# Kernel tuning notes

Hardware: AMD Instinct MI355X
Metric: run time of the kernel (lower is better)

The kernel has to match this reference:

```python
import jax, jax.numpy as jnp
import numpy as np

NUM_HEADS = 8


def setup_inputs() -> dict:
    key = jax.random.key(0)
    ks = jax.random.split(key, 8)
    B, C, H, W = 8, 512, 64, 64
    s = 1.0 / np.sqrt(C)
    return {
        "guide": jax.random.normal(ks[0], (B, C), dtype=jnp.float32),
        "hidden_rep": jax.random.normal(ks[1], (B, C, H, W), dtype=jnp.float32),
        "Wq": jax.random.normal(ks[2], (C, C), dtype=jnp.float32) * s,
        "bq": jnp.zeros((C,), dtype=jnp.float32),
        "Wk": jax.random.normal(ks[3], (C, C), dtype=jnp.float32) * s,
        "bk": jnp.zeros((C,), dtype=jnp.float32),
        "Wv": jax.random.normal(ks[4], (C, C), dtype=jnp.float32) * s,
        "bv": jnp.zeros((C,), dtype=jnp.float32),
    }


def reference(guide, hidden_rep, Wq, bq, Wk, bk, Wv, bv):
    B, C, H, W = hidden_rep.shape
    nh = NUM_HEADS
    d = C // nh
    scale = 1.0 / (d ** 0.5)

    # hidden_rep: [B,C,H,W] -> [B, HW, C] (token-major, matching torch permute+reshape)
    hr = hidden_rep.transpose(0, 2, 3, 1).reshape(B, H * W, C)

    # guide is broadcast identically over all HW positions in the original;
    # the linear commutes with the broadcast, so compute once then broadcast.
    q_row = guide @ Wq.T + bq                                   # [B, C]
    q_tok = jnp.broadcast_to(q_row[:, None, :], (B, H * W, C))  # [B, HW, C]
    k_tok = hr @ Wk.T + bk                                      # [B, HW, C]
    v_tok = hr @ Wv.T + bv                                      # [B, HW, C]

    # Faithful replication of torch split_heads: view [B,HW,C] as [B,nh,d,H,W]
    # (this scrambles spatial/channel axes exactly as the original does),
    # then permute to [B, nh, H, W, d].
    def split_heads(x):
        return x.reshape(B, nh, d, H, W).transpose(0, 1, 3, 4, 2)

    q = split_heads(q_tok)  # [B, nh, H, W, d]
    k = split_heads(k_tok)
    v = split_heads(v_tok)

    # Row-wise attention: softmax over the width axis only.
    scores = jnp.einsum('bnhqd,bnhkd->bnhqk', q, k) * scale  # [B, nh, H, W, W]
    weights = jax.nn.softmax(scores, axis=-1)
    attended = jnp.einsum('bnhqk,bnhkd->bnhqd', weights, v)  # [B, nh, H, W, d]

    # permute(0,1,4,2,3) -> [B, nh, d, H, W] -> [B, C, H, W]
    return attended.transpose(0, 1, 4, 2, 3).reshape(B, C, H, W)
```

## Files before the change

kernel.cpp:

```cpp
#include <hip/hip_runtime.h>
#include <hip/hip_bf16.h>
#include <stdint.h>


typedef __attribute__((ext_vector_type(8))) short bf16x8_t;
typedef __attribute__((ext_vector_type(4))) float f32x4_t;

__device__ __forceinline__ unsigned short f2bf(float f) {
  unsigned int u = __float_as_uint(f);
  u += 0x7FFFu + ((u >> 16) & 1u);
  return (unsigned short)(u >> 16);
}

__device__ __forceinline__ void gload16(const void* g, void* lds) {
  __builtin_amdgcn_global_load_lds(
      (const __attribute__((address_space(1))) unsigned int*)g,
      (__attribute__((address_space(3))) unsigned int*)lds, 16, 0, 0);
}

__global__ __launch_bounds__(256) void k_trans(const float* __restrict__ hid,
                                               unsigned short* __restrict__ XT,
                                               float* __restrict__ hrsum,
                                               const float* __restrict__ Wv,
                                               unsigned short* __restrict__ Wvb) {
  int bid = blockIdx.x;
  int tid = threadIdx.x;
  if (bid >= 512) {
    int blk = bid - 512;
#pragma unroll
    for (int i = 0; i < 16; ++i) {
      int idx = blk * 4096 + i * 256 + tid;
      float4 v = ((const float4*)Wv)[idx];
      ushort4 o;
      o.x = f2bf(v.x); o.y = f2bf(v.y); o.z = f2bf(v.z); o.w = f2bf(v.w);
      ((ushort4*)Wvb)[idx] = o;
    }
    return;
  }
  int cb = bid & 7, n = (bid >> 3) & 7, b = bid >> 6;
  __shared__ float T[64][65];
  __shared__ float hsred[64][8];

  for (int i = tid; i < 512; i += 256) ((float*)hsred)[i] = 0.f;

  float part[4][4];
#pragma unroll
  for (int m = 0; m < 4; ++m)
#pragma unroll
    for (int i = 0; i < 4; ++i) part[m][i] = 0.f;

  const int f4 = tid & 15;
  const int r0 = tid >> 4;
  const float* srcbase = hid + (size_t)(b * 512 + cb * 64) * 4096 + n * 512;
  unsigned short* xtbase = XT + (size_t)(b * 8 + n) * 512 * 512 + cb * 64;

  for (int jc = 0; jc < 8; ++jc) {
    __syncthreads();
#pragma unroll
    for (int m = 0; m < 4; ++m) {
      int r = r0 + 16 * m;
      float4 v = *(const float4*)(srcbase + (size_t)r * 4096 + jc * 64 + f4 * 4);
      T[r][f4 * 4 + 0] = v.x;  T[r][f4 * 4 + 1] = v.y;
      T[r][f4 * 4 + 2] = v.z;  T[r][f4 * 4 + 3] = v.w;
      part[m][0] += v.x; part[m][1] += v.y; part[m][2] += v.z; part[m][3] += v.w;
    }
    __syncthreads();
#pragma unroll
    for (int p = 0; p < 2; ++p) {
      int jl = (tid >> 3) + p * 32;
      int o = tid & 7;
      unsigned short t0 = f2bf(T[o * 8 + 0][jl]);
      unsigned short t1 = f2bf(T[o * 8 + 1][jl]);
      unsigned short t2 = f2bf(T[o * 8 + 2][jl]);
      unsigned short t3 = f2bf(T[o * 8 + 3][jl]);
      unsigned short t4 = f2bf(T[o * 8 + 4][jl]);
      unsigned short t5 = f2bf(T[o * 8 + 5][jl]);
      unsigned short t6 = f2bf(T[o * 8 + 6][jl]);
      unsigned short t7 = f2bf(T[o * 8 + 7][jl]);
      uint4 pk;
      pk.x = (unsigned)t0 | ((unsigned)t1 << 16);
      pk.y = (unsigned)t2 | ((unsigned)t3 << 16);
      pk.z = (unsigned)t4 | ((unsigned)t5 << 16);
      pk.w = (unsigned)t6 | ((unsigned)t7 << 16);
      *(uint4*)(xtbase + (size_t)(jc * 64 + jl) * 512 + o * 8) = pk;
    }
  }
  __syncthreads();
  {
    int gbase = (tid & 1) * 4;
#pragma unroll
    for (int m = 0; m < 4; ++m) {
      int r = r0 + 16 * m;
#pragma unroll
      for (int i = 0; i < 4; ++i) atomicAdd(&hsred[r][gbase + i], part[m][i]);
    }
  }
  __syncthreads();
  float* hout = hrsum + (size_t)(b * 8 + n) * 8 * 512 + cb * 64;
  for (int i = tid; i < 512; i += 256) {
    int g = i >> 6, r = i & 63;
    hout[(size_t)g * 512 + r] = hsred[r][g];
  }
}

__global__ __launch_bounds__(256) void k_k2(const float* __restrict__ hrsum,
                                            const float* __restrict__ Wk,
                                            const float* __restrict__ bk,
                                            const float* __restrict__ guide,
                                            const float* __restrict__ Wq,
                                            const float* __restrict__ bq,
                                            float* __restrict__ K2,
                                            float* __restrict__ qs) {
  int bid = blockIdx.x;
  int rt = bid >> 4, ct = bid & 15;
  bool isQ = (rt == 16);
  const float* A = isQ ? guide : (hrsum + (size_t)rt * 32 * 512);
  const float* Bm = isQ ? Wq : Wk;
  int arows = isQ ? 8 : 32;
  int tid = threadIdx.x;
  __shared__ float Ah[32][36];
  __shared__ float Bh[32][36];
  int r = tid >> 3, f = tid & 7;
  int oy = (tid >> 4) * 2, ox = (tid & 15) * 2;
  float a00 = 0.f, a01 = 0.f, a10 = 0.f, a11 = 0.f;

  for (int kc = 0; kc < 16; ++kc) {
    __syncthreads();
    float4 av = (r < arows) ? *(const float4*)(A + (size_t)r * 512 + kc * 32 + f * 4)
                            : make_float4(0.f, 0.f, 0.f, 0.f);
    *(float4*)(&Ah[r][f * 4]) = av;
    float4 bv = *(const float4*)(Bm + (size_t)(ct * 32 + r) * 512 + kc * 32 + f * 4);
    *(float4*)(&Bh[r][f * 4]) = bv;
    __syncthreads();
#pragma unroll
    for (int kk = 0; kk < 32; kk += 4) {
      float4 x0 = *(float4*)(&Ah[oy][kk]);
      float4 x1 = *(float4*)(&Ah[oy + 1][kk]);
      float4 y0 = *(float4*)(&Bh[ox][kk]);
      float4 y1 = *(float4*)(&Bh[ox + 1][kk]);
      a00 += x0.x * y0.x + x0.y * y0.y + x0.z * y0.z + x0.w * y0.w;
      a01 += x0.x * y1.x + x0.y * y1.y + x0.z * y1.z + x0.w * y1.w;
      a10 += x1.x * y0.x + x1.y * y0.y + x1.z * y0.z + x1.w * y0.w;
      a11 += x1.x * y1.x + x1.y * y1.y + x1.z * y1.z + x1.w * y1.w;
    }
  }
  int c0 = ct * 32 + ox;
  if (!isQ) {
    int row0 = rt * 32 + oy;
    K2[(size_t)row0 * 512 + c0]           = a00 + 64.f * bk[c0];
    K2[(size_t)row0 * 512 + c0 + 1]       = a01 + 64.f * bk[c0 + 1];
    K2[(size_t)(row0 + 1) * 512 + c0]     = a10 + 64.f * bk[c0];
    K2[(size_t)(row0 + 1) * 512 + c0 + 1] = a11 + 64.f * bk[c0 + 1];
  } else if (oy < 8) {
    const float scale = 0.125f;
    qs[(size_t)oy * 512 + c0]           = (a00 + bq[c0]) * scale;
    qs[(size_t)oy * 512 + c0 + 1]       = (a01 + bq[c0 + 1]) * scale;
    qs[(size_t)(oy + 1) * 512 + c0]     = (a10 + bq[c0]) * scale;
    qs[(size_t)(oy + 1) * 512 + c0 + 1] = (a11 + bq[c0 + 1]) * scale;
  }
}

__global__ __launch_bounds__(512, 2) void k_fused(
    const unsigned short* __restrict__ XT, const unsigned short* __restrict__ Wvb,
    const float* __restrict__ K2, const float* __restrict__ qs,
    const float* __restrict__ bv, float* __restrict__ out) {
  int bid = blockIdx.x;
  int g = bid & 7, slab = bid >> 3;
  int n = slab & 7, b = slab >> 3;
  int tid = threadIdx.x;
  int w = tid >> 6, l = tid & 63;
  int l15 = l & 15, l4 = l >> 4, lr = l >> 3, lc = l & 7;

  __shared__ __align__(16) unsigned char smem[151552];
  float* K2l = (float*)(smem + 147456);
  float* bvl = (float*)(smem + 149504);

  const unsigned swzel = (unsigned)((lc ^ lr) << 3);
  const unsigned short* bsrc = XT + (size_t)slab * 512 * 512;
  const int myArow = w * 64;
  const int myBrow = w * 8;

  if (w < 2) {
    gload16(K2 + (size_t)(slab * 8 + g) * 512 + w * 256 + l * 4,
            (unsigned char*)K2l + w * 1024);
  } else if (w < 4) {
    gload16(bv + (w - 2) * 256 + l * 4, (unsigned char*)bvl + (w - 2) * 1024);
  }

#define STAGE(kc, buf)                                                          \
  do {                                                                          \
    unsigned char* Ab_ = smem + (buf)*65536;                                    \
    unsigned char* Bb_ = smem + 131072 + (buf)*8192;                            \
    _Pragma("unroll")                                                           \
    for (int i_ = 0; i_ < 8; ++i_) {                                            \
      int r_ = myArow + i_ * 8 + lr;                                            \
      gload16(Wvb + (size_t)r_ * 512 + (kc)*64 + swzel,                         \
              Ab_ + (myArow + i_ * 8) * 128);                                   \
    }                                                                           \
    int rb_ = myBrow + lr;                                                      \
    gload16(bsrc + (size_t)(8 * rb_ + g) * 512 + (kc)*64 + swzel,               \
            Bb_ + myBrow * 128);                                                \
  } while (0)

  f32x4_t acc[4][4];
#pragma unroll
  for (int i = 0; i < 4; ++i)
#pragma unroll
    for (int j = 0; j < 4; ++j) acc[i][j] = (f32x4_t){0.f, 0.f, 0.f, 0.f};

  STAGE(0, 0);
  STAGE(1, 1);

#pragma unroll
  for (int kc = 0; kc < 8; ++kc) {
    if (kc < 7) asm volatile("s_waitcnt vmcnt(9)" ::: "memory");
    else        asm volatile("s_waitcnt vmcnt(0)" ::: "memory");
    __builtin_amdgcn_s_barrier();
    {
      unsigned char* Ab = smem + (kc & 1) * 65536;
      unsigned char* Bb = smem + 131072 + (kc & 1) * 8192;
#pragma unroll
      for (int ks = 0; ks < 2; ++ks) {
        unsigned colb = (unsigned)(ks * 64 + l4 * 16);
        bf16x8_t af[4], bfr[4];
#pragma unroll
        for (int mt = 0; mt < 4; ++mt) {
          unsigned row = (unsigned)(myArow + mt * 16 + l15);
          af[mt] = *(const bf16x8_t*)(Ab + row * 128 + (colb ^ ((row & 7) << 4)));
        }
#pragma unroll
        for (int nt = 0; nt < 4; ++nt) {
          unsigned row = (unsigned)(nt * 16 + l15);
          bfr[nt] = *(const bf16x8_t*)(Bb + row * 128 + (colb ^ ((row & 7) << 4)));
        }
#pragma unroll
        for (int mt = 0; mt < 4; ++mt)
#pragma unroll
          for (int nt = 0; nt < 4; ++nt)
            acc[mt][nt] = __builtin_amdgcn_mfma_f32_16x16x32_bf16(
                af[mt], bfr[nt], acc[mt][nt], 0, 0, 0);
      }
    }
    __builtin_amdgcn_s_barrier();
    if (kc < 6) {
      if ((kc & 1) == 0) STAGE(kc + 2, 0);
      else               STAGE(kc + 2, 1);
    }
  }
#undef STAGE

  unsigned char* Vl = smem;
#pragma unroll
  for (int nt = 0; nt < 4; ++nt) {
    unsigned dd = (unsigned)(nt * 16 + l15);
    unsigned swz = (dd & 7) << 4;
#pragma unroll
    for (int mt = 0; mt < 4; ++mt) {
      int c0 = w * 64 + mt * 16 + l4 * 4;
      float4 bq4 = *(const float4*)(bvl + c0);
      float v0 = acc[mt][nt][0] + bq4.x;
      float v1 = acc[mt][nt][1] + bq4.y;
      float v2 = acc[mt][nt][2] + bq4.z;
      float v3 = acc[mt][nt][3] + bq4.w;
      uint2 pk;
      pk.x = (unsigned)f2bf(v0) | ((unsigned)f2bf(v1) << 16);
      pk.y = (unsigned)f2bf(v2) | ((unsigned)f2bf(v3) << 16);
      *(uint2*)(Vl + dd * 1024 + (((unsigned)(c0 * 2)) ^ swz)) = pk;
    }
  }
  __syncthreads();

  const int e = w;
  float alpha = qs[(size_t)b * 512 + e * 64 + l];
  float mmax = -3.0e38f;
#pragma unroll 8
  for (int kk = 0; kk < 64; ++kk)
    mmax = fmaxf(mmax, alpha * K2l[e * 64 + kk]);
  float ssum = 0.f;
#pragma unroll 8
  for (int kk = 0; kk < 64; ++kk)
    ssum += __expf(alpha * K2l[e * 64 + kk] - mmax);
  float inv = 1.0f / ssum;

  f32x4_t acc2[4][4];
#pragma unroll
  for (int i = 0; i < 4; ++i)
#pragma unroll
    for (int j = 0; j < 4; ++j) acc2[i][j] = (f32x4_t){0.f, 0.f, 0.f, 0.f};

#pragma unroll
  for (int ks = 0; ks < 2; ++ks) {
    bf16x8_t va[4];
#pragma unroll
    for (int mt = 0; mt < 4; ++mt) {
      unsigned dd = (unsigned)(mt * 16 + l15);
      unsigned colb = (unsigned)(e * 128 + ks * 64 + l4 * 16);
      va[mt] = *(const bf16x8_t*)(Vl + dd * 1024 + (colb ^ ((dd & 7) << 4)));
    }
    int kk0 = ks * 32 + l4 * 8;
    float4 be0 = *(float4*)(&K2l[e * 64 + kk0]);
    float4 be1 = *(float4*)(&K2l[e * 64 + kk0 + 4]);
    bf16x8_t pb[4];
#pragma unroll
    for (int nt = 0; nt < 4; ++nt) {
      int qq = nt * 16 + l15;
      float aq = __shfl(alpha, qq);
      float mq = __shfl(mmax, qq);
      float iq = __shfl(inv, qq);
      bf16x8_t p;
      p[0] = (short)f2bf(__expf(aq * be0.x - mq) * iq);
      p[1] = (short)f2bf(__expf(aq * be0.y - mq) * iq);
      p[2] = (short)f2bf(__expf(aq * be0.z - mq) * iq);
      p[3] = (short)f2bf(__expf(aq * be0.w - mq) * iq);
      p[4] = (short)f2bf(__expf(aq * be1.x - mq) * iq);
      p[5] = (short)f2bf(__expf(aq * be1.y - mq) * iq);
      p[6] = (short)f2bf(__expf(aq * be1.z - mq) * iq);
      p[7] = (short)f2bf(__expf(aq * be1.w - mq) * iq);
      pb[nt] = p;
    }
#pragma unroll
    for (int mt = 0; mt < 4; ++mt)
#pragma unroll
      for (int nt = 0; nt < 4; ++nt)
        acc2[mt][nt] = __builtin_amdgcn_mfma_f32_16x16x32_bf16(
            va[mt], pb[nt], acc2[mt][nt], 0, 0, 0);
  }

#pragma unroll
  for (int mt = 0; mt < 4; ++mt) {
#pragma unroll
    for (int r = 0; r < 4; ++r) {
      int dd = mt * 16 + l4 * 4 + r;
      size_t base = (((size_t)(b * 512 + n * 64 + dd)) * 64 + (g * 8 + e)) * 64;
#pragma unroll
      for (int nt = 0; nt < 4; ++nt)
        out[base + nt * 16 + l15] = acc2[mt][nt][r];
    }
  }
}

extern "C" void kernel_launch(void* const* d_in, const int* in_sizes, int n_in,
                              void* d_out, int out_size, void* d_ws, size_t ws_size,
                              hipStream_t stream) {
  const float* guide = (const float*)d_in[0];
  const float* hid   = (const float*)d_in[1];
  const float* Wq    = (const float*)d_in[2];
  const float* bq    = (const float*)d_in[3];
  const float* Wk    = (const float*)d_in[4];
  const float* bk    = (const float*)d_in[5];
  const float* Wv    = (const float*)d_in[6];
  const float* bv    = (const float*)d_in[7];
  float* out = (float*)d_out;

  char* ws = (char*)d_ws;
  unsigned short* XT  = (unsigned short*)(ws);
  unsigned short* Wvb = (unsigned short*)(ws + 33554432);
  float* hrsum        = (float*)(ws + 34078720);
  float* K2           = (float*)(ws + 35127296);
  float* qs           = (float*)(ws + 36175872);

  k_trans<<<528, 256, 0, stream>>>(hid, XT, hrsum, Wv, Wvb);
  k_k2<<<272, 256, 0, stream>>>(hrsum, Wk, bk, guide, Wq, bq, K2, qs);
  k_fused<<<512, 512, 0, stream>>>(XT, Wvb, K2, qs, bv, out);
}
```

Baseline: 96.20 us.

## Load Wv fragments directly to registers, shrink LDS, remap blocks per XCD

The fused V-projection/attention kernel no longer stages the 512x64 Wv tile through LDS. Each wave reads its A fragments straight from global memory into double-buffered registers, and only the small XT tile is staged in LDS. LDS drops from about 148KB to 80KB and launch bounds rise to 4 blocks per CU, to raise occupancy. Blocks are remapped so slabs are grouped per XCD for L2 locality, and the softmax max becomes a closed-form wave reduction using min/max of beta with shuffles, replacing LDS loops. The risk is heavier register pressure and global-load latency for Wv reads that are no longer shared through LDS.

```diff
diff --git a/kernel.cpp b/kernel.cpp
--- a/kernel.cpp
+++ b/kernel.cpp
@@ -160,47 +160,39 @@
   }
 }
 
-__global__ __launch_bounds__(512, 2) void k_fused(
+__global__ __launch_bounds__(512, 4) void k_fused(
     const unsigned short* __restrict__ XT, const unsigned short* __restrict__ Wvb,
     const float* __restrict__ K2, const float* __restrict__ qs,
     const float* __restrict__ bv, float* __restrict__ out) {
-  int bid = blockIdx.x;
-  int g = bid & 7, slab = bid >> 3;
+  int p = blockIdx.x;
+  int xcd = p & 7, idx = p >> 3;
+  int slab = xcd * 8 + (idx & 7);
+  int g = idx >> 3;
   int n = slab & 7, b = slab >> 3;
+
   int tid = threadIdx.x;
   int w = tid >> 6, l = tid & 63;
   int l15 = l & 15, l4 = l >> 4, lr = l >> 3, lc = l & 7;
 
-  __shared__ __align__(16) unsigned char smem[151552];
-  float* K2l = (float*)(smem + 147456);
-  float* bvl = (float*)(smem + 149504);
+  __shared__ __align__(16) unsigned char smem[81920];
+  unsigned char* Vp = smem + 16384 + w * 8192;
 
   const unsigned swzel = (unsigned)((lc ^ lr) << 3);
   const unsigned short* bsrc = XT + (size_t)slab * 512 * 512;
-  const int myArow = w * 64;
-  const int myBrow = w * 8;
-
-  if (w < 2) {
-    gload16(K2 + (size_t)(slab * 8 + g) * 512 + w * 256 + l * 4,
-            (unsigned char*)K2l + w * 1024);
-  } else if (w < 4) {
-    gload16(bv + (w - 2) * 256 + l * 4, (unsigned char*)bvl + (w - 2) * 1024);
-  }
-
-#define STAGE(kc, buf)                                                          \
-  do {                                                                          \
-    unsigned char* Ab_ = smem + (buf)*65536;                                    \
-    unsigned char* Bb_ = smem + 131072 + (buf)*8192;                            \
-    _Pragma("unroll")                                                           \
-    for (int i_ = 0; i_ < 8; ++i_) {                                            \
-      int r_ = myArow + i_ * 8 + lr;                                            \
-      gload16(Wvb + (size_t)r_ * 512 + (kc)*64 + swzel,                         \
-              Ab_ + (myArow + i_ * 8) * 128);                                   \
-    }                                                                           \
-    int rb_ = myBrow + lr;                                                      \
-    gload16(bsrc + (size_t)(8 * rb_ + g) * 512 + (kc)*64 + swzel,               \
-            Bb_ + myBrow * 128);                                                \
-  } while (0)
+  const unsigned short* wbase = Wvb + (size_t)(w * 64 + l15) * 512 + l4 * 8;
+  const int brow = 8 * (w * 8 + lr) + g;
+
+  float alpha = qs[(size_t)b * 512 + w * 64 + l];
+  float beta  = K2[(size_t)(slab * 8 + g) * 512 + w * 64 + l];
+  float bvreg = bv[w * 64 + l];
+
+  gload16(bsrc + (size_t)brow * 512 + 0 * 64 + swzel, smem + 0 * 8192 + w * 1024);
+  gload16(bsrc + (size_t)brow * 512 + 1 * 64 + swzel, smem + 1 * 8192 + w * 1024);
+
+  bf16x8_t af[2][4];
+#pragma unroll
+  for (int mt = 0; mt < 4; ++mt)
+    af[0][mt] = *(const bf16x8_t*)(wbase + mt * 16 * 512);
 
   f32x4_t acc[4][4];
 #pragma unroll
@@ -208,78 +200,76 @@
 #pragma unroll
     for (int j = 0; j < 4; ++j) acc[i][j] = (f32x4_t){0.f, 0.f, 0.f, 0.f};
 
-  STAGE(0, 0);
-  STAGE(1, 1);
-
 #pragma unroll
   for (int kc = 0; kc < 8; ++kc) {
-    if (kc < 7) asm volatile("s_waitcnt vmcnt(9)" ::: "memory");
-    else        asm volatile("s_waitcnt vmcnt(0)" ::: "memory");
+    if (kc < 7) asm volatile("s_waitcnt vmcnt(5)" ::: "memory");
+    else        asm volatile("s_waitcnt vmcnt(4)" ::: "memory");
     __builtin_amdgcn_s_barrier();
-    {
-      unsigned char* Ab = smem + (kc & 1) * 65536;
-      unsigned char* Bb = smem + 131072 + (kc & 1) * 8192;
-#pragma unroll
-      for (int ks = 0; ks < 2; ++ks) {
-        unsigned colb = (unsigned)(ks * 64 + l4 * 16);
-        bf16x8_t af[4], bfr[4];
-#pragma unroll
-        for (int mt = 0; mt < 4; ++mt) {
-          unsigned row = (unsigned)(myArow + mt * 16 + l15);
-          af[mt] = *(const bf16x8_t*)(Ab + row * 128 + (colb ^ ((row & 7) << 4)));
-        }
-#pragma unroll
-        for (int nt = 0; nt < 4; ++nt) {
-          unsigned row = (unsigned)(nt * 16 + l15);
-          bfr[nt] = *(const bf16x8_t*)(Bb + row * 128 + (colb ^ ((row & 7) << 4)));
-        }
+    asm volatile("" ::: "memory");
+    unsigned char* Bb = smem + (kc & 1) * 8192;
+#pragma unroll
+    for (int ks = 0; ks < 2; ++ks) {
+      const int s = kc * 2 + ks;
+      if (s < 15) {
 #pragma unroll
         for (int mt = 0; mt < 4; ++mt)
-#pragma unroll
-          for (int nt = 0; nt < 4; ++nt)
-            acc[mt][nt] = __builtin_amdgcn_mfma_f32_16x16x32_bf16(
-                af[mt], bfr[nt], acc[mt][nt], 0, 0, 0);
+          af[(s + 1) & 1][mt] =
+              *(const bf16x8_t*)(wbase + mt * 16 * 512 + (s + 1) * 32);
       }
-    }
+      bf16x8_t bfr[4];
+#pragma unroll
+      for (int nt = 0; nt < 4; ++nt) {
+        unsigned row = (unsigned)(nt * 16 + l15);
+        bfr[nt] = *(const bf16x8_t*)(Bb + row * 128 +
+                                     ((unsigned)(ks * 64 + l4 * 16) ^ ((row & 7) << 4)));
+      }
+      __builtin_amdgcn_s_setprio(1);
+#pragma unroll
+      for (int mt = 0; mt < 4; ++mt)
+#pragma unroll
+        for (int nt = 0; nt < 4; ++nt)
+          acc[mt][nt] = __builtin_amdgcn_mfma_f32_16x16x32_bf16(
+              af[s & 1][mt], bfr[nt], acc[mt][nt], 0, 0, 0);
+      __builtin_amdgcn_s_setprio(0);
+    }
+    asm volatile("" ::: "memory");
     __builtin_amdgcn_s_barrier();
-    if (kc < 6) {
-      if ((kc & 1) == 0) STAGE(kc + 2, 0);
-      else               STAGE(kc + 2, 1);
-    }
-  }
-#undef STAGE
-
-  unsigned char* Vl = smem;
-#pragma unroll
-  for (int nt = 0; nt < 4; ++nt) {
-    unsigned dd = (unsigned)(nt * 16 + l15);
-    unsigned swz = (dd & 7) << 4;
-#pragma unroll
-    for (int mt = 0; mt < 4; ++mt) {
-      int c0 = w * 64 + mt * 16 + l4 * 4;
-      float4 bq4 = *(const float4*)(bvl + c0);
-      float v0 = acc[mt][nt][0] + bq4.x;
-      float v1 = acc[mt][nt][1] + bq4.y;
-      float v2 = acc[mt][nt][2] + bq4.z;
-      float v3 = acc[mt][nt][3] + bq4.w;
+    asm volatile("" ::: "memory");
+    if (kc < 6)
+      gload16(bsrc + (size_t)brow * 512 + (kc + 2) * 64 + swzel,
+              smem + (kc & 1) * 8192 + w * 1024);
+  }
+
+#pragma unroll
+  for (int mt = 0; mt < 4; ++mt) {
+    float bq0 = __shfl(bvreg, mt * 16 + l4 * 4 + 0);
+    float bq1 = __shfl(bvreg, mt * 16 + l4 * 4 + 1);
+    float bq2 = __shfl(bvreg, mt * 16 + l4 * 4 + 2);
+    float bq3 = __shfl(bvreg, mt * 16 + l4 * 4 + 3);
+#pragma unroll
+    for (int nt = 0; nt < 4; ++nt) {
+      unsigned dd = (unsigned)(nt * 16 + l15);
       uint2 pk;
-      pk.x = (unsigned)f2bf(v0) | ((unsigned)f2bf(v1) << 16);
-      pk.y = (unsigned)f2bf(v2) | ((unsigned)f2bf(v3) << 16);
-      *(uint2*)(Vl + dd * 1024 + (((unsigned)(c0 * 2)) ^ swz)) = pk;
-    }
-  }
-  __syncthreads();
-
-  const int e = w;
-  float alpha = qs[(size_t)b * 512 + e * 64 + l];
-  float mmax = -3.0e38f;
-#pragma unroll 8
-  for (int kk = 0; kk < 64; ++kk)
-    mmax = fmaxf(mmax, alpha * K2l[e * 64 + kk]);
+      pk.x = (unsigned)f2bf(acc[mt][nt][0] + bq0) |
+             ((unsigned)f2bf(acc[mt][nt][1] + bq1) << 16);
+      pk.y = (unsigned)f2bf(acc[mt][nt][2] + bq2) |
+             ((unsigned)f2bf(acc[mt][nt][3] + bq3) << 16);
+      *(uint2*)(Vp + dd * 128 +
+                ((unsigned)(mt * 32 + l4 * 8) ^ ((dd & 7) << 4))) = pk;
+    }
+  }
+
+  float bmax = beta, bmin = beta;
+#pragma unroll
+  for (int o = 32; o >= 1; o >>= 1) {
+    bmax = fmaxf(bmax, __shfl_xor(bmax, o));
+    bmin = fminf(bmin, __shfl_xor(bmin, o));
+  }
+  float m = alpha >= 0.f ? alpha * bmax : alpha * bmin;
   float ssum = 0.f;
 #pragma unroll 8
   for (int kk = 0; kk < 64; ++kk)
-    ssum += __expf(alpha * K2l[e * 64 + kk] - mmax);
+    ssum += __expf(fmaf(alpha, __shfl(beta, kk), -m));
   float inv = 1.0f / ssum;
 
   f32x4_t acc2[4][4];
@@ -294,29 +284,24 @@
 #pragma unroll
     for (int mt = 0; mt < 4; ++mt) {
       unsigned dd = (unsigned)(mt * 16 + l15);
-      unsigned colb = (unsigned)(e * 128 + ks * 64 + l4 * 16);
-      va[mt] = *(const bf16x8_t*)(Vl + dd * 1024 + (colb ^ ((dd & 7) << 4)));
-    }
-    int kk0 = ks * 32 + l4 * 8;
-    float4 be0 = *(float4*)(&K2l[e * 64 + kk0]);
-    float4 be1 = *(float4*)(&K2l[e * 64 + kk0 + 4]);
+      va[mt] = *(const bf16x8_t*)(Vp + dd * 128 +
+                ((unsigned)(ks * 64 + l4 * 16) ^ ((dd & 7) << 4)));
+    }
+    float bvv[8];
+#pragma unroll
+    for (int i = 0; i < 8; ++i) bvv[i] = __shfl(beta, ks * 32 + l4 * 8 + i);
     bf16x8_t pb[4];
 #pragma unroll
     for (int nt = 0; nt < 4; ++nt) {
       int qq = nt * 16 + l15;
       float aq = __shfl(alpha, qq);
-      float mq = __shfl(mmax, qq);
+      float mq = __shfl(m, qq);
       float iq = __shfl(inv, qq);
-      bf16x8_t p;
-      p[0] = (short)f2bf(__expf(aq * be0.x - mq) * iq);
-      p[1] = (short)f2bf(__expf(aq * be0.y - mq) * iq);
-      p[2] = (short)f2bf(__expf(aq * be0.z - mq) * iq);
-      p[3] = (short)f2bf(__expf(aq * be0.w - mq) * iq);
-      p[4] = (short)f2bf(__expf(aq * be1.x - mq) * iq);
-      p[5] = (short)f2bf(__expf(aq * be1.y - mq) * iq);
-      p[6] = (short)f2bf(__expf(aq * be1.z - mq) * iq);
-      p[7] = (short)f2bf(__expf(aq * be1.w - mq) * iq);
-      pb[nt] = p;
+      bf16x8_t pp;
+#pragma unroll
+      for (int i = 0; i < 8; ++i)
+        pp[i] = (short)f2bf(__expf(fmaf(aq, bvv[i], -mq)) * iq);
+      pb[nt] = pp;
     }
 #pragma unroll
     for (int mt = 0; mt < 4; ++mt)
@@ -331,7 +316,7 @@
 #pragma unroll
     for (int r = 0; r < 4; ++r) {
       int dd = mt * 16 + l4 * 4 + r;
-      size_t base = (((size_t)(b * 512 + n * 64 + dd)) * 64 + (g * 8 + e)) * 64;
+      size_t base = (((size_t)(b * 512 + n * 64 + dd)) * 64 + (g * 8 + w)) * 64;
 #pragma unroll
       for (int nt = 0; nt < 4; ++nt)
         out[base + nt * 16 + l15] = acc2[mt][nt][r];
```

New measurement: 95.63 us. No clear change (-0.6%).
